# Optimization experiments

Hardware: AMD Instinct MI355X
Metric: run time of the kernel (lower is better)

Reference implementation:

```python
import jax, jax.numpy as jnp
import numpy as np

C, H, N, B, L = 1, 512, 64, 16, 2048  # n_channels, n_heads, d_kernel, batch, seq_len


def setup_inputs() -> dict:
    key = jax.random.key(0)
    k1, k2 = jax.random.split(key)
    u = jax.random.normal(k1, (B, C * H, L), dtype=jnp.float32)
    k = jax.random.normal(k2, (C, H, N), dtype=jnp.float32)
    return {"u": u, "k": k}


def _l1_normalize(x, axis):
    # torch.linalg.norm(x, ord=1, dim=axis, keepdim=True): vector 1-norm along `axis`
    return x / jnp.sum(jnp.abs(x), axis=axis, keepdims=True)


def _forward(u, k):
    c, h, n = k.shape
    bsz, d, l = u.shape  # d == c*h
    dt = u.dtype
    # Shift matrix A: A[:, :, 1:, :-1] = I  (companion-style shift)
    A = jnp.zeros((c, h, n, n), dtype=dt).at[:, :, 1:, :-1].set(jnp.eye(n - 1, dtype=dt))
    # b = e1 broadcast to (c, h, n)
    b_vec = jnp.zeros((c, h, n), dtype=dt).at[:, :, 0].set(1.0)
    # closed-loop: k_norm = L1-normalize(clamp(k, 1/16, 1)); A_cl = L1-normalize(A + b k^T)
    k_norm = _l1_normalize(jnp.clip(k, 1.0 / 16.0, 1.0), axis=2)
    BK = jnp.einsum('chi,chj->chij', b_vec, k_norm)
    M = _l1_normalize(A + BK, axis=2)

    # Krylov recurrence: f[i] = k . (M^i b), i = 0..l-1
    def step(x, _):
        f_i = jnp.einsum('chn,chn->ch', k, x)
        x_next = jnp.einsum('chij,chj->chi', M, x)
        return x_next, f_i

    _, f = jax.lax.scan(step, b_vec, None, length=l)  # f: (l, c, h)
    f = jnp.moveaxis(f, 0, -1)  # (c, h, l)

    # Causal FFT convolution of u (b, c, h, l) with filter f (c, h, l)
    n_fft = 2 * l
    uf = jnp.fft.rfft(u.reshape(bsz, c, h, l), n=n_fft)
    ff = jnp.fft.rfft(f, n=n_fft)
    y = jnp.fft.irfft(uf * ff[None], n=n_fft)[..., :l]
    return y.reshape(bsz, c * h, l)


def reference(u, k):
    return _forward(u, k)
```

## Files before the change

kernel.cpp:

```cpp
#include <hip/hip_runtime.h>


namespace {

constexpr int kH = 512;
constexpr int kL = 2048;

typedef __attribute__((ext_vector_type(8))) short bf16x8;
typedef __attribute__((ext_vector_type(4))) float f32x4;

#define MFMA(A, B, C) __builtin_amdgcn_mfma_f32_16x16x32_bf16((A), (B), (C), 0, 0, 0)

__device__ inline unsigned int cvt_pk_bf16(float lo, float hi) {
  unsigned int r;
  asm("v_cvt_pk_bf16_f32 %0, %1, %2" : "=v"(r) : "v"(lo), "v"(hi));
  return r;
}

union B8U4 { bf16x8 v; unsigned int u[4]; };

__device__ inline void cvt_split8(const f32x4 a, const f32x4 b, bf16x8& fh, bf16x8& fl) {
  B8U4 H, L;
  float x[8];
  #pragma unroll
  for (int j = 0; j < 4; ++j) { x[j] = a[j]; x[4 + j] = b[j]; }
  #pragma unroll
  for (int d = 0; d < 4; ++d) {
    const float x0 = x[2 * d], x1 = x[2 * d + 1];
    const unsigned int hp = cvt_pk_bf16(x0, x1);
    const float h0 = __uint_as_float(hp << 16);
    const float h1 = __uint_as_float(hp & 0xFFFF0000u);
    H.u[d] = hp;
    L.u[d] = cvt_pk_bf16(x0 - h0, x1 - h1);
  }
  fh = H.v; fl = L.v;
}

__device__ inline void gen_frag(const float* tp, int n0, bf16x8& fh, bf16x8& fl) {
  float t[8];
  #pragma unroll
  for (int j = 0; j < 8; ++j) {
    const int n = n0 - j;
    t[j] = (n >= 0 && n < 127) ? tp[n] : 0.0f;
  }
  const f32x4 a = {t[0], t[1], t[2], t[3]};
  const f32x4 b = {t[4], t[5], t[6], t[7]};
  cvt_split8(a, b, fh, fl);
}

__device__ inline void gen_fragB(const float* tp, int base, bf16x8& fh, bf16x8& fl) {
  float t[8];
  #pragma unroll
  for (int j = 0; j < 8; ++j) t[j] = tp[base + j];
  const f32x4 a = {t[0], t[1], t[2], t[3]};
  const f32x4 b = {t[4], t[5], t[6], t[7]};
  cvt_split8(a, b, fh, fl);
}

__global__ __launch_bounds__(256, 2)
void ssm_mfma_kernel(const float* __restrict__ u,
                     const float* __restrict__ kin,
                     float* __restrict__ y) {
  const int h    = blockIdx.x;
  const int tid  = threadIdx.x;
  const int wid  = tid >> 6;
  const int lane = tid & 63;
  const int ln16 = lane & 15;
  const int quad = lane >> 4;

  __shared__ alignas(16) char pool[69632];
  auto taps = (float (*)[128]) (pool);
  float* wPad = (float*) (pool + 1536);
  auto stA = (float (*)[68]) (pool + 2048);
  auto stB = (float (*)[68]) (pool + 19456);
  auto scr = (float (*)[68]) (pool + 2048 + wid * 4352);
  auto sT  = (bf16x8 (*)[2][2][64]) (pool + 36864);
  auto g1T = (bf16x8 (*)[2][2][64]) (pool + 53248);
  auto g2T = (bf16x8 (*)[2][2][64]) (pool + 19456);

  const int cb = 8 * wid;
  const float* ub = u + ((size_t)ln16 * kH + h) * kL + 8 * quad;
  float* yb = y + ((size_t)ln16 * kH + h) * kL;
  f32x4 uv[4];
  #pragma unroll
  for (int i = 0; i < 4; ++i)
    uv[i] = *(const f32x4*)(ub + 64 * cb + 32 * (i >> 1) + 4 * (i & 1));

  if (wid == 0) {
    const float kv = kin[h * 64 + lane];
    const float kc = fminf(fmaxf(kv, 0.0625f), 1.0f);
    float ks = kc;
    #pragma unroll
    for (int off = 32; off >= 1; off >>= 1) ks += __shfl_xor(ks, off);
    const float kn = kc / ks;
    const float cc = 1.0f / (1.0f + kn);
    float pp = cc;
    #pragma unroll
    for (int off = 1; off < 64; off <<= 1) {
      const float t = __shfl_up(pp, off);
      if (lane >= off) pp *= t;
    }
    float Pe = __shfl_up(pp, 1);
    if (lane == 0) Pe = 1.0f;
    const float wv = (lane < 63) ? (kn * cc * Pe) : Pe;
    const float gv = kv * Pe;
    float sv = (lane == 0) ? 1.0f : 0.0f;
    for (int rr = 0; rr < 63; ++rr) {
      const float s0 = __shfl(sv, rr);
      const float cf = __shfl(wv, lane - 1 - rr);
      if (lane > rr) sv = fmaf(cf, s0, sv);
    }
    taps[0][lane] = 0.0f;
    taps[1][lane] = 0.0f;
    const float gn = __shfl(gv, lane + 1);
    taps[2][lane] = (lane < 63) ? gn : 0.0f;
    taps[2][64 + lane] = 0.0f;
    taps[0][63 + lane] = sv;
    taps[1][63 + lane] = gv;
    if (lane == 0) { taps[0][127] = 0.0f; taps[1][127] = 0.0f; }
    wPad[lane] = wv;
    wPad[64 + lane] = 0.0f;
  }
  __syncthreads();

  {
    bf16x8 sH[4][2], sL[4][2];
    #pragma unroll
    for (int mt = 0; mt < 4; ++mt) {
      #pragma unroll
      for (int tk = 0; tk < 2; ++tk) {
        const int n0 = 16 * mt + ln16 - (32 * tk + 8 * quad) + 63;
        gen_frag(taps[0], n0, sH[mt][tk], sL[mt][tk]);
      }
    }
    #pragma unroll
    for (int mt = 0; mt < 4; ++mt) {
      f32x4 acc = {0.f, 0.f, 0.f, 0.f};
      #pragma unroll
      for (int tk = 0; tk < 2; ++tk) {
        const int base = 8 * quad + 32 * tk - (16 * wid + ln16) + 63;
        bf16x8 bh, bl;
        gen_fragB(wPad, base, bh, bl);
        acc = MFMA(sH[mt][tk], bh, acc);
        acc = MFMA(sH[mt][tk], bl, acc);
        acc = MFMA(sL[mt][tk], bh, acc);
        acc = MFMA(sL[mt][tk], bl, acc);
      }
      #pragma unroll
      for (int r = 0; r < 4; ++r)
        stA[16 * mt + 4 * quad + r][16 * wid + ln16] = acc[r];
    }
    #pragma unroll
    for (int tk = 0; tk < 2; ++tk) {
      const int n0 = 16 * wid + ln16 - (32 * tk + 8 * quad) + 63;
      bf16x8 fh, fl;
      gen_frag(taps[0], n0, fh, fl);
      sT[wid][tk][0][lane] = fh;  sT[wid][tk][1][lane] = fl;
      gen_frag(taps[2], n0, fh, fl);
      g1T[wid][tk][0][lane] = fh; g1T[wid][tk][1][lane] = fl;
    }
  }
  __syncthreads();

  bf16x8 aH[4][2], aL[4][2];
  #pragma unroll
  for (int mt = 0; mt < 4; ++mt) {
    #pragma unroll
    for (int tk = 0; tk < 2; ++tk) {
      const int row = 16 * mt + ln16, k0 = 32 * tk + 8 * quad;
      cvt_split8(*(const f32x4*)&stA[row][k0], *(const f32x4*)&stA[row][k0 + 4],
                 aH[mt][tk], aL[mt][tk]);
    }
  }
  #pragma unroll
  for (int mt = 0; mt < 4; ++mt) {
    f32x4 acc = {0.f, 0.f, 0.f, 0.f};
    #pragma unroll
    for (int tk = 0; tk < 2; ++tk) {
      float t[8];
      #pragma unroll
      for (int j = 0; j < 8; ++j)
        t[j] = stA[8 * quad + 32 * tk + j][16 * wid + ln16];
      const f32x4 a = {t[0], t[1], t[2], t[3]};
      const f32x4 b = {t[4], t[5], t[6], t[7]};
      bf16x8 bh, bl;
      cvt_split8(a, b, bh, bl);
      acc = MFMA(aH[mt][tk], bh, acc);
      acc = MFMA(aH[mt][tk], bl, acc);
      acc = MFMA(aL[mt][tk], bh, acc);
      acc = MFMA(aL[mt][tk], bl, acc);
    }
    #pragma unroll
    for (int r = 0; r < 4; ++r)
      stB[16 * mt + 4 * quad + r][16 * wid + ln16] = acc[r];
  }
  __syncthreads();

  #pragma unroll
  for (int sq = 0; sq < 2; ++sq) {
    float (*src)[68] = (sq == 0) ? stB : stA;
    float (*dst)[68] = (sq == 0) ? stA : stB;
    #pragma unroll
    for (int mt = 0; mt < 4; ++mt) {
      bf16x8 rh[2], rl[2];
      #pragma unroll
      for (int tk = 0; tk < 2; ++tk) {
        const int row = 16 * mt + ln16, k0 = 32 * tk + 8 * quad;
        cvt_split8(*(const f32x4*)&src[row][k0], *(const f32x4*)&src[row][k0 + 4],
                   rh[tk], rl[tk]);
      }
      f32x4 acc = {0.f, 0.f, 0.f, 0.f};
      #pragma unroll
      for (int tk = 0; tk < 2; ++tk) {
        float t[8];
        #pragma unroll
        for (int j = 0; j < 8; ++j)
          t[j] = src[8 * quad + 32 * tk + j][16 * wid + ln16];
        const f32x4 a = {t[0], t[1], t[2], t[3]};
        const f32x4 b = {t[4], t[5], t[6], t[7]};
        bf16x8 bh, bl;
        cvt_split8(a, b, bh, bl);
        acc = MFMA(rh[tk], bh, acc);
        acc = MFMA(rh[tk], bl, acc);
        acc = MFMA(rl[tk], bh, acc);
        acc = MFMA(rl[tk], bl, acc);
      }
      #pragma unroll
      for (int r = 0; r < 4; ++r)
        dst[16 * mt + 4 * quad + r][16 * wid + ln16] = acc[r];
    }
    __syncthreads();
  }

  bf16x8 pH[2], pL[2];
  {
    bf16x8 z;
    #pragma unroll
    for (int j = 0; j < 8; ++j) z[j] = 0;
    pH[0] = z; pH[1] = z; pL[0] = z; pL[1] = z;
  }

  #pragma unroll 1
  for (int i = 0; i < 8; ++i) {
    bf16x8 uH[2], uL[2];
    cvt_split8(uv[0], uv[1], uH[0], uL[0]);
    cvt_split8(uv[2], uv[3], uH[1], uL[1]);
    const int tn = 64 * ((i < 7) ? (cb + i + 1) : cb);
    #pragma unroll
    for (int q = 0; q < 4; ++q)
      uv[q] = *(const f32x4*)(ub + tn + 32 * (q >> 1) + 4 * (q & 1));

    f32x4 acc[4];
    #pragma unroll
    for (int mt = 0; mt < 4; ++mt) acc[mt] = (f32x4){0.f, 0.f, 0.f, 0.f};
    #pragma unroll
    for (int mt = 0; mt < 4; ++mt) {
      #pragma unroll
      for (int tk = 0; tk < 2; ++tk) {
        acc[mt] = MFMA(aH[mt][tk], pH[tk], acc[mt]);
        acc[mt] = MFMA(aH[mt][tk], pL[tk], acc[mt]);
        acc[mt] = MFMA(aL[mt][tk], pH[tk], acc[mt]);
      }
      #pragma unroll
      for (int tk = 0; tk < 2; ++tk) {
        const bf16x8 th = sT[mt][tk][0][lane];
        const bf16x8 tl = sT[mt][tk][1][lane];
        acc[mt] = MFMA(th, uH[tk], acc[mt]);
        acc[mt] = MFMA(th, uL[tk], acc[mt]);
        acc[mt] = MFMA(tl, uH[tk], acc[mt]);
      }
    }
    #pragma unroll
    for (int mt = 0; mt < 4; ++mt)
      *(f32x4*)&scr[ln16][16 * mt + 4 * quad] = acc[mt];
    asm volatile("s_waitcnt lgkmcnt(0)" ::: "memory");
    __builtin_amdgcn_sched_barrier(0);
    #pragma unroll
    for (int tk = 0; tk < 2; ++tk) {
      const int k0 = 8 * quad + 32 * tk;
      cvt_split8(*(const f32x4*)&scr[ln16][k0], *(const f32x4*)&scr[ln16][k0 + 4],
                 pH[tk], pL[tk]);
    }
  }

  asm volatile("s_waitcnt lgkmcnt(0)" ::: "memory");
  __builtin_amdgcn_s_barrier();
  asm volatile("" ::: "memory");

  bf16x8 c0H[2], c0L[2];
  f32x4 sac1[4], sac2[4];
  {
    float (*s0)[68] = (float (*)[68])(pool + 2048);
    float (*s1)[68] = (float (*)[68])(pool + 2048 + 4352);
    float (*s2)[68] = (float (*)[68])(pool + 2048 + 2 * 4352);
    if (wid == 1) {
      #pragma unroll
      for (int tk = 0; tk < 2; ++tk) {
        const int k0 = 8 * quad + 32 * tk;
        cvt_split8(*(const f32x4*)&s0[ln16][k0], *(const f32x4*)&s0[ln16][k0 + 4],
                   pH[tk], pL[tk]);
      }
    } else if (wid == 2) {
      #pragma unroll
      for (int tk = 0; tk < 2; ++tk) {
        const int k0 = 8 * quad + 32 * tk;
        cvt_split8(*(const f32x4*)&s0[ln16][k0], *(const f32x4*)&s0[ln16][k0 + 4],
                   c0H[tk], c0L[tk]);
      }
      #pragma unroll
      for (int mt = 0; mt < 4; ++mt)
        sac1[mt] = *(const f32x4*)&s1[ln16][16 * mt + 4 * quad];
    } else if (wid == 3) {
      #pragma unroll
      for (int tk = 0; tk < 2; ++tk) {
        const int k0 = 8 * quad + 32 * tk;
        cvt_split8(*(const f32x4*)&s0[ln16][k0], *(const f32x4*)&s0[ln16][k0 + 4],
                   c0H[tk], c0L[tk]);
      }
      #pragma unroll
      for (int mt = 0; mt < 4; ++mt) {
        sac1[mt] = *(const f32x4*)&s1[ln16][16 * mt + 4 * quad];
        sac2[mt] = *(const f32x4*)&s2[ln16][16 * mt + 4 * quad];
      }
    }
  }
  asm volatile("s_waitcnt lgkmcnt(0)" ::: "memory");
  __builtin_amdgcn_s_barrier();
  asm volatile("" ::: "memory");

  if (wid == 0) {
    bf16x8 z;
    #pragma unroll
    for (int j = 0; j < 8; ++j) z[j] = 0;
    pH[0] = z; pH[1] = z; pL[0] = z; pL[1] = z;
  } else if (wid >= 2) {
    #pragma unroll
    for (int mt = 0; mt < 4; ++mt) {
      bf16x8 a8h[2], a8l[2];
      #pragma unroll
      for (int tk = 0; tk < 2; ++tk) {
        const int row = 16 * mt + ln16, k0 = 32 * tk + 8 * quad;
        cvt_split8(*(const f32x4*)&stB[row][k0], *(const f32x4*)&stB[row][k0 + 4],
                   a8h[tk], a8l[tk]);
      }
      #pragma unroll
      for (int tk = 0; tk < 2; ++tk) {
        sac1[mt] = MFMA(a8h[tk], c0H[tk], sac1[mt]);
        sac1[mt] = MFMA(a8h[tk], c0L[tk], sac1[mt]);
        sac1[mt] = MFMA(a8l[tk], c0H[tk], sac1[mt]);
        sac1[mt] = MFMA(a8l[tk], c0L[tk], sac1[mt]);
      }
    }
    #pragma unroll
    for (int mt = 0; mt < 4; ++mt)
      *(f32x4*)&scr[ln16][16 * mt + 4 * quad] = sac1[mt];
    asm volatile("s_waitcnt lgkmcnt(0)" ::: "memory");
    __builtin_amdgcn_sched_barrier(0);
    #pragma unroll
    for (int tk = 0; tk < 2; ++tk) {
      const int k0 = 8 * quad + 32 * tk;
      cvt_split8(*(const f32x4*)&scr[ln16][k0], *(const f32x4*)&scr[ln16][k0 + 4],
                 pH[tk], pL[tk]);
    }
    if (wid == 3) {
      #pragma unroll
      for (int mt = 0; mt < 4; ++mt) {
        bf16x8 a8h[2], a8l[2];
        #pragma unroll
        for (int tk = 0; tk < 2; ++tk) {
          const int row = 16 * mt + ln16, k0 = 32 * tk + 8 * quad;
          cvt_split8(*(const f32x4*)&stB[row][k0], *(const f32x4*)&stB[row][k0 + 4],
                     a8h[tk], a8l[tk]);
        }
        #pragma unroll
        for (int tk = 0; tk < 2; ++tk) {
          sac2[mt] = MFMA(a8h[tk], pH[tk], sac2[mt]);
          sac2[mt] = MFMA(a8h[tk], pL[tk], sac2[mt]);
          sac2[mt] = MFMA(a8l[tk], pH[tk], sac2[mt]);
          sac2[mt] = MFMA(a8l[tk], pL[tk], sac2[mt]);
        }
      }
      #pragma unroll
      for (int mt = 0; mt < 4; ++mt)
        *(f32x4*)&scr[ln16][16 * mt + 4 * quad] = sac2[mt];
      asm volatile("s_waitcnt lgkmcnt(0)" ::: "memory");
      __builtin_amdgcn_sched_barrier(0);
      #pragma unroll
      for (int tk = 0; tk < 2; ++tk) {
        const int k0 = 8 * quad + 32 * tk;
        cvt_split8(*(const f32x4*)&scr[ln16][k0], *(const f32x4*)&scr[ln16][k0 + 4],
                   pH[tk], pL[tk]);
      }
    }
  }
  asm volatile("s_waitcnt lgkmcnt(0)" ::: "memory");
  __builtin_amdgcn_s_barrier();
  asm volatile("" ::: "memory");

  #pragma unroll
  for (int tk = 0; tk < 2; ++tk) {
    const int n0 = 16 * wid + ln16 - (32 * tk + 8 * quad) + 63;
    bf16x8 fh, fl;
    gen_frag(taps[1], n0, fh, fl);
    g2T[wid][tk][0][lane] = fh;  g2T[wid][tk][1][lane] = fl;
  }
  asm volatile("s_waitcnt lgkmcnt(0)" ::: "memory");
  __builtin_amdgcn_s_barrier();
  asm volatile("" ::: "memory");

  #pragma unroll 1
  for (int i = 0; i < 8; ++i) {
    bf16x8 uH[2], uL[2];
    cvt_split8(uv[0], uv[1], uH[0], uL[0]);
    cvt_split8(uv[2], uv[3], uH[1], uL[1]);
    const int tn = 64 * ((i < 7) ? (cb + i + 1) : cb);
    #pragma unroll
    for (int q = 0; q < 4; ++q)
      uv[q] = *(const f32x4*)(ub + tn + 32 * (q >> 1) + 4 * (q & 1));

    f32x4 accR[4], accY[4];
    #pragma unroll
    for (int mt = 0; mt < 4; ++mt) {
      accR[mt] = (f32x4){0.f, 0.f, 0.f, 0.f};
      accY[mt] = (f32x4){0.f, 0.f, 0.f, 0.f};
    }
    #pragma unroll
    for (int mt = 0; mt < 4; ++mt) {
      #pragma unroll
      for (int tk = 0; tk < 2; ++tk) {
        accR[mt] = MFMA(aH[mt][tk], pH[tk], accR[mt]);
        accR[mt] = MFMA(aH[mt][tk], pL[tk], accR[mt]);
        accR[mt] = MFMA(aL[mt][tk], pH[tk], accR[mt]);
      }
      #pragma unroll
      for (int tk = 0; tk < 2; ++tk) {
        const bf16x8 th = sT[mt][tk][0][lane];
        const bf16x8 tl = sT[mt][tk][1][lane];
        accR[mt] = MFMA(th, uH[tk], accR[mt]);
        accR[mt] = MFMA(th, uL[tk], accR[mt]);
        accR[mt] = MFMA(tl, uH[tk], accR[mt]);
      }
    }
    #pragma unroll
    for (int mt = 0; mt < 4; ++mt)
      *(f32x4*)&scr[ln16][16 * mt + 4 * quad] = accR[mt];
    #pragma unroll
    for (int mt = 0; mt < 4; ++mt) {
      #pragma unroll
      for (int tk = 0; tk < 2; ++tk) {
        const bf16x8 gh = g1T[mt][tk][0][lane];
        const bf16x8 gl = g1T[mt][tk][1][lane];
        accY[mt] = MFMA(gh, pH[tk], accY[mt]);
        accY[mt] = MFMA(gh, pL[tk], accY[mt]);
        accY[mt] = MFMA(gl, pH[tk], accY[mt]);
      }
    }
    asm volatile("s_waitcnt lgkmcnt(0)" ::: "memory");
    __builtin_amdgcn_sched_barrier(0);
    #pragma unroll
    for (int tk = 0; tk < 2; ++tk) {
      const int k0 = 8 * quad + 32 * tk;
      cvt_split8(*(const f32x4*)&scr[ln16][k0], *(const f32x4*)&scr[ln16][k0 + 4],
                 pH[tk], pL[tk]);
    }
    #pragma unroll
    for (int mt = 0; mt < 4; ++mt) {
      #pragma unroll
      for (int tk = 0; tk < 2; ++tk) {
        const bf16x8 gh = g2T[mt][tk][0][lane];
        const bf16x8 gl = g2T[mt][tk][1][lane];
        accY[mt] = MFMA(gh, pH[tk], accY[mt]);
        accY[mt] = MFMA(gh, pL[tk], accY[mt]);
        accY[mt] = MFMA(gl, pH[tk], accY[mt]);
      }
      *(f32x4*)(yb + 64 * (cb + i) + 16 * mt + 4 * quad) = accY[mt];
    }
  }
}

}

extern "C" void kernel_launch(void* const* d_in, const int* in_sizes, int n_in,
                              void* d_out, int out_size, void* d_ws, size_t ws_size,
                              hipStream_t stream) {
  const float* u  = (const float*)d_in[0];
  const float* kk = (const float*)d_in[1];
  if (n_in >= 2 && in_sizes[0] < in_sizes[1]) {
    const float* t = u; u = kk; kk = t;
  }
  float* yy = (float*)d_out;
  hipLaunchKernelGGL(ssm_mfma_kernel, dim3(kH), dim3(256), 0, stream, u, kk, yy);
}
```

Before: 148.0 us.

## Precompute combined output matrices so final chunk pass needs one dependent step

The setup phase now precomputes G1+G2·A and G2·S, the products of the output tap matrices with the transition matrices. The final pass computes each output chunk directly from the previous state and the current input, so the second state-dependent MFMA batch no longer waits on the state update and its scratch round-trip. The S fragments are now kept in registers instead of being re-read from LDS in the hot loops. The cost is extra setup MFMAs and barriers, higher register pressure, and slightly different rounding from the changed association.

Result: no change. 148.7 us (+0.5%).

```diff
diff --git a/kernel.cpp b/kernel.cpp
--- a/kernel.cpp
+++ b/kernel.cpp
@@ -74,9 +74,8 @@
   auto stA = (float (*)[68]) (pool + 2048);
   auto stB = (float (*)[68]) (pool + 19456);
   auto scr = (float (*)[68]) (pool + 2048 + wid * 4352);
-  auto sT  = (bf16x8 (*)[2][2][64]) (pool + 36864);
-  auto g1T = (bf16x8 (*)[2][2][64]) (pool + 53248);
-  auto g2T = (bf16x8 (*)[2][2][64]) (pool + 19456);
+  auto G2ST = (bf16x8 (*)[2][2][64]) (pool + 36864);
+  auto GpT  = (bf16x8 (*)[2][2][64]) (pool + 53248);
 
   const int cb = 8 * wid;
   const float* ub = u + ((size_t)ln16 * kH + h) * kL + 8 * quad;
@@ -124,45 +123,44 @@
   __syncthreads();
 
   {
-    bf16x8 sH[4][2], sL[4][2];
-    #pragma unroll
-    for (int mt = 0; mt < 4; ++mt) {
+    bf16x8 wbh[2], wbl[2], sbh[2], sbl[2];
+    #pragma unroll
+    for (int tk = 0; tk < 2; ++tk) {
+      const int base = 8 * quad + 32 * tk - (16 * wid + ln16) + 63;
+      gen_fragB(wPad, base, wbh[tk], wbl[tk]);
+      gen_fragB(taps[0], base, sbh[tk], sbl[tk]);
+    }
+    #pragma unroll
+    for (int mt = 0; mt < 4; ++mt) {
+      bf16x8 xh[2], xl[2], gh[2], gl[2];
       #pragma unroll
       for (int tk = 0; tk < 2; ++tk) {
         const int n0 = 16 * mt + ln16 - (32 * tk + 8 * quad) + 63;
-        gen_frag(taps[0], n0, sH[mt][tk], sL[mt][tk]);
-      }
-    }
-    #pragma unroll
-    for (int mt = 0; mt < 4; ++mt) {
-      f32x4 acc = {0.f, 0.f, 0.f, 0.f};
-      #pragma unroll
-      for (int tk = 0; tk < 2; ++tk) {
-        const int base = 8 * quad + 32 * tk - (16 * wid + ln16) + 63;
-        bf16x8 bh, bl;
-        gen_fragB(wPad, base, bh, bl);
-        acc = MFMA(sH[mt][tk], bh, acc);
-        acc = MFMA(sH[mt][tk], bl, acc);
-        acc = MFMA(sL[mt][tk], bh, acc);
-        acc = MFMA(sL[mt][tk], bl, acc);
-      }
-      #pragma unroll
-      for (int r = 0; r < 4; ++r)
-        stA[16 * mt + 4 * quad + r][16 * wid + ln16] = acc[r];
-    }
-    #pragma unroll
-    for (int tk = 0; tk < 2; ++tk) {
-      const int n0 = 16 * wid + ln16 - (32 * tk + 8 * quad) + 63;
-      bf16x8 fh, fl;
-      gen_frag(taps[0], n0, fh, fl);
-      sT[wid][tk][0][lane] = fh;  sT[wid][tk][1][lane] = fl;
-      gen_frag(taps[2], n0, fh, fl);
-      g1T[wid][tk][0][lane] = fh; g1T[wid][tk][1][lane] = fl;
+        gen_frag(taps[0], n0, xh[tk], xl[tk]);
+        gen_frag(taps[1], n0, gh[tk], gl[tk]);
+      }
+      f32x4 accA = {0.f, 0.f, 0.f, 0.f};
+      f32x4 accG = {0.f, 0.f, 0.f, 0.f};
+      #pragma unroll
+      for (int tk = 0; tk < 2; ++tk) {
+        accA = MFMA(xh[tk], wbh[tk], accA);
+        accA = MFMA(xh[tk], wbl[tk], accA);
+        accA = MFMA(xl[tk], wbh[tk], accA);
+        accA = MFMA(xl[tk], wbl[tk], accA);
+        accG = MFMA(gh[tk], sbh[tk], accG);
+        accG = MFMA(gh[tk], sbl[tk], accG);
+        accG = MFMA(gl[tk], sbh[tk], accG);
+      }
+      #pragma unroll
+      for (int r = 0; r < 4; ++r) {
+        stA[16 * mt + 4 * quad + r][16 * wid + ln16] = accA[r];
+        stB[16 * mt + 4 * quad + r][16 * wid + ln16] = accG[r];
+      }
     }
   }
   __syncthreads();
 
-  bf16x8 aH[4][2], aL[4][2];
+  bf16x8 aH[4][2], aL[4][2], sH[4][2], sL[4][2];
   #pragma unroll
   for (int mt = 0; mt < 4; ++mt) {
     #pragma unroll
@@ -170,11 +168,22 @@
       const int row = 16 * mt + ln16, k0 = 32 * tk + 8 * quad;
       cvt_split8(*(const f32x4*)&stA[row][k0], *(const f32x4*)&stA[row][k0 + 4],
                  aH[mt][tk], aL[mt][tk]);
-    }
-  }
-  #pragma unroll
-  for (int mt = 0; mt < 4; ++mt) {
-    f32x4 acc = {0.f, 0.f, 0.f, 0.f};
+      const int n0 = 16 * mt + ln16 - (32 * tk + 8 * quad) + 63;
+      gen_frag(taps[0], n0, sH[mt][tk], sL[mt][tk]);
+    }
+  }
+  #pragma unroll
+  for (int tk = 0; tk < 2; ++tk) {
+    const int row = 16 * wid + ln16, k0 = 32 * tk + 8 * quad;
+    bf16x8 fh, fl;
+    cvt_split8(*(const f32x4*)&stB[row][k0], *(const f32x4*)&stB[row][k0 + 4],
+               fh, fl);
+    G2ST[wid][tk][0][lane] = fh;  G2ST[wid][tk][1][lane] = fl;
+  }
+  __syncthreads();
+
+  {
+    bf16x8 abh[2], abl[2];
     #pragma unroll
     for (int tk = 0; tk < 2; ++tk) {
       float t[8];
@@ -183,16 +192,68 @@
         t[j] = stA[8 * quad + 32 * tk + j][16 * wid + ln16];
       const f32x4 a = {t[0], t[1], t[2], t[3]};
       const f32x4 b = {t[4], t[5], t[6], t[7]};
-      bf16x8 bh, bl;
-      cvt_split8(a, b, bh, bl);
-      acc = MFMA(aH[mt][tk], bh, acc);
-      acc = MFMA(aH[mt][tk], bl, acc);
-      acc = MFMA(aL[mt][tk], bh, acc);
-      acc = MFMA(aL[mt][tk], bl, acc);
-    }
-    #pragma unroll
-    for (int r = 0; r < 4; ++r)
-      stB[16 * mt + 4 * quad + r][16 * wid + ln16] = acc[r];
+      cvt_split8(a, b, abh[tk], abl[tk]);
+    }
+    #pragma unroll
+    for (int mt = 0; mt < 4; ++mt) {
+      bf16x8 gh[2], gl[2];
+      #pragma unroll
+      for (int tk = 0; tk < 2; ++tk) {
+        const int n0 = 16 * mt + ln16 - (32 * tk + 8 * quad) + 63;
+        gen_frag(taps[1], n0, gh[tk], gl[tk]);
+      }
+      f32x4 acc = {0.f, 0.f, 0.f, 0.f};
+      #pragma unroll
+      for (int tk = 0; tk < 2; ++tk) {
+        acc = MFMA(gh[tk], abh[tk], acc);
+        acc = MFMA(gh[tk], abl[tk], acc);
+        acc = MFMA(gl[tk], abh[tk], acc);
+      }
+      #pragma unroll
+      for (int r = 0; r < 4; ++r) {
+        const int i = 16 * mt + 4 * quad + r, j = 16 * wid + ln16;
+        stB[i][j] = acc[r] + taps[2][(i - j) + 63];
+      }
+    }
+  }
+  __syncthreads();
+
+  #pragma unroll
+  for (int tk = 0; tk < 2; ++tk) {
+    const int row = 16 * wid + ln16, k0 = 32 * tk + 8 * quad;
+    bf16x8 fh, fl;
+    cvt_split8(*(const f32x4*)&stB[row][k0], *(const f32x4*)&stB[row][k0 + 4],
+               fh, fl);
+    GpT[wid][tk][0][lane] = fh;  GpT[wid][tk][1][lane] = fl;
+  }
+  __syncthreads();
+
+  {
+    bf16x8 abh[2], abl[2];
+    #pragma unroll
+    for (int tk = 0; tk < 2; ++tk) {
+      float t[8];
+      #pragma unroll
+      for (int j = 0; j < 8; ++j)
+        t[j] = stA[8 * quad + 32 * tk + j][16 * wid + ln16];
+      const f32x4 a = {t[0], t[1], t[2], t[3]};
+      const f32x4 b = {t[4], t[5], t[6], t[7]};
+      cvt_split8(a, b, abh[tk], abl[tk]);
+    }
+    #pragma unroll
+    for (int mt = 0; mt < 4; ++mt) {
+      f32x4 acc = {0.f, 0.f, 0.f, 0.f};
+      #pragma unroll
+      for (int tk = 0; tk < 2; ++tk) {
+        acc = MFMA(aH[mt][tk], abh[tk], acc);
+        acc = MFMA(aH[mt][tk], abl[tk], acc);
+        acc = MFMA(aL[mt][tk], abh[tk], acc);
+        acc = MFMA(aL[mt][tk], abl[tk], acc);
+      }
+      #pragma unroll
+      for (int r = 0; r < 4; ++r)
+        stB[16 * mt + 4 * quad + r][16 * wid + ln16] = acc[r];
+    }
   }
   __syncthreads();
 
@@ -263,11 +324,9 @@
       }
       #pragma unroll
       for (int tk = 0; tk < 2; ++tk) {
-        const bf16x8 th = sT[mt][tk][0][lane];
-        const bf16x8 tl = sT[mt][tk][1][lane];
-        acc[mt] = MFMA(th, uH[tk], acc[mt]);
-        acc[mt] = MFMA(th, uL[tk], acc[mt]);
-        acc[mt] = MFMA(tl, uH[tk], acc[mt]);
+        acc[mt] = MFMA(sH[mt][tk], uH[tk], acc[mt]);
+        acc[mt] = MFMA(sH[mt][tk], uL[tk], acc[mt]);
+        acc[mt] = MFMA(sL[mt][tk], uH[tk], acc[mt]);
       }
     }
     #pragma unroll
@@ -397,17 +456,6 @@
   __builtin_amdgcn_s_barrier();
   asm volatile("" ::: "memory");
 
-  #pragma unroll
-  for (int tk = 0; tk < 2; ++tk) {
-    const int n0 = 16 * wid + ln16 - (32 * tk + 8 * quad) + 63;
-    bf16x8 fh, fl;
-    gen_frag(taps[1], n0, fh, fl);
-    g2T[wid][tk][0][lane] = fh;  g2T[wid][tk][1][lane] = fl;
-  }
-  asm volatile("s_waitcnt lgkmcnt(0)" ::: "memory");
-  __builtin_amdgcn_s_barrier();
-  asm volatile("" ::: "memory");
-
   #pragma unroll 1
   for (int i = 0; i < 8; ++i) {
     bf16x8 uH[2], uL[2];
@@ -418,12 +466,9 @@
     for (int q = 0; q < 4; ++q)
       uv[q] = *(const f32x4*)(ub + tn + 32 * (q >> 1) + 4 * (q & 1));
 
-    f32x4 accR[4], accY[4];
-    #pragma unroll
-    for (int mt = 0; mt < 4; ++mt) {
-      accR[mt] = (f32x4){0.f, 0.f, 0.f, 0.f};
-      accY[mt] = (f32x4){0.f, 0.f, 0.f, 0.f};
-    }
+    f32x4 accR[4];
+    #pragma unroll
+    for (int mt = 0; mt < 4; ++mt) accR[mt] = (f32x4){0.f, 0.f, 0.f, 0.f};
     #pragma unroll
     for (int mt = 0; mt < 4; ++mt) {
       #pragma unroll
@@ -434,46 +479,48 @@
       }
       #pragma unroll
       for (int tk = 0; tk < 2; ++tk) {
-        const bf16x8 th = sT[mt][tk][0][lane];
-        const bf16x8 tl = sT[mt][tk][1][lane];
-        accR[mt] = MFMA(th, uH[tk], accR[mt]);
-        accR[mt] = MFMA(th, uL[tk], accR[mt]);
-        accR[mt] = MFMA(tl, uH[tk], accR[mt]);
+        accR[mt] = MFMA(sH[mt][tk], uH[tk], accR[mt]);
+        accR[mt] = MFMA(sH[mt][tk], uL[tk], accR[mt]);
+        accR[mt] = MFMA(sL[mt][tk], uH[tk], accR[mt]);
       }
     }
     #pragma unroll
     for (int mt = 0; mt < 4; ++mt)
       *(f32x4*)&scr[ln16][16 * mt + 4 * quad] = accR[mt];
-    #pragma unroll
-    for (int mt = 0; mt < 4; ++mt) {
-      #pragma unroll
-      for (int tk = 0; tk < 2; ++tk) {
-        const bf16x8 gh = g1T[mt][tk][0][lane];
-        const bf16x8 gl = g1T[mt][tk][1][lane];
+
+    f32x4 accY[4];
+    #pragma unroll
+    for (int mt = 0; mt < 4; ++mt) accY[mt] = (f32x4){0.f, 0.f, 0.f, 0.f};
+    #pragma unroll
+    for (int mt = 0; mt < 4; ++mt) {
+      #pragma unroll
+      for (int tk = 0; tk < 2; ++tk) {
+        const bf16x8 gh = GpT[mt][tk][0][lane];
+        const bf16x8 gl = GpT[mt][tk][1][lane];
         accY[mt] = MFMA(gh, pH[tk], accY[mt]);
         accY[mt] = MFMA(gh, pL[tk], accY[mt]);
         accY[mt] = MFMA(gl, pH[tk], accY[mt]);
       }
-    }
-    asm volatile("s_waitcnt lgkmcnt(0)" ::: "memory");
-    __builtin_amdgcn_sched_barrier(0);
-    #pragma unroll
-    for (int tk = 0; tk < 2; ++tk) {
-      const int k0 = 8 * quad + 32 * tk;
-      cvt_split8(*(const f32x4*)&scr[ln16][k0], *(const f32x4*)&scr[ln16][k0 + 4],
-                 pH[tk], pL[tk]);
-    }
-    #pragma unroll
-    for (int mt = 0; mt < 4; ++mt) {
-      #pragma unroll
-      for (int tk = 0; tk < 2; ++tk) {
-        const bf16x8 gh = g2T[mt][tk][0][lane];
-        const bf16x8 gl = g2T[mt][tk][1][lane];
-        accY[mt] = MFMA(gh, pH[tk], accY[mt]);
-        accY[mt] = MFMA(gh, pL[tk], accY[mt]);
-        accY[mt] = MFMA(gl, pH[tk], accY[mt]);
+      #pragma unroll
+      for (int tk = 0; tk < 2; ++tk) {
+        const bf16x8 gh = G2ST[mt][tk][0][lane];
+        const bf16x8 gl = G2ST[mt][tk][1][lane];
+        accY[mt] = MFMA(gh, uH[tk], accY[mt]);
+        accY[mt] = MFMA(gh, uL[tk], accY[mt]);
+        accY[mt] = MFMA(gl, uH[tk], accY[mt]);
       }
       *(f32x4*)(yb + 64 * (cb + i) + 16 * mt + 4 * quad) = accY[mt];
+    }
+
+    if (i < 7) {
+      asm volatile("s_waitcnt lgkmcnt(0)" ::: "memory");
+      __builtin_amdgcn_sched_barrier(0);
+      #pragma unroll
+      for (int tk = 0; tk < 2; ++tk) {
+        const int k0 = 8 * quad + 32 * tk;
+        cvt_split8(*(const f32x4*)&scr[ln16][k0], *(const f32x4*)&scr[ln16][k0 + 4],
+                   pH[tk], pL[tk]);
+      }
     }
   }
 }
```
